# Kernel tuning notes

Hardware: AMD Instinct MI355X
Metric: run time of the kernel (lower is better)

The kernel has to match this reference:

```python
import jax, jax.numpy as jnp
import numpy as np

NEG_SLOPE = 0.2

def setup_inputs() -> dict:
    key = jax.random.key(0)
    k1, k2, k3, k4 = jax.random.split(key, 4)
    N, K, C_IN, C_OUT = 8192, 4, 512, 512
    inputs = jax.random.normal(k1, (N, C_IN), dtype=jnp.float32)
    adj_set = jax.random.uniform(k2, (K, N, N), dtype=jnp.float32)
    att = jax.random.uniform(k3, (K,), dtype=jnp.float32)
    # xavier_uniform for w
    limit = float(np.sqrt(6.0 / (C_IN + C_OUT)))
    w = jax.random.uniform(k4, (C_IN, C_OUT), minval=-limit, maxval=limit, dtype=jnp.float32)
    b = jnp.zeros((C_OUT,), dtype=jnp.float32)
    return {"inputs": inputs, "adj_set": adj_set, "att": att, "w": w, "b": b}

def reference(inputs, adj_set, att, w, b):
    # support: [N, C_out]
    support = inputs @ w + b
    # residual=True path: outputs = sum_i att[i] * (adj_i @ support)
    #                             = (sum_i att[i] * adj_i) @ support
    combined_adj = jnp.einsum('k,knm->nm', att, adj_set)  # [N, N]
    outputs = combined_adj @ support                       # [N, C_out]
    # LeakyReLU(negative_slope=0.2)
    return jnp.where(outputs >= 0, outputs, NEG_SLOPE * outputs)
```

## Files before the change

kernel.cpp:

```cpp
#include <hip/hip_runtime.h>

#define LP  40
#define LPB 40

typedef __attribute__((ext_vector_type(8))) short short8;
typedef __attribute__((ext_vector_type(4))) short short4t;
typedef __attribute__((ext_vector_type(4))) float f32x4;

__device__ __forceinline__ short f2bf(float f) {
  unsigned u = __builtin_bit_cast(unsigned, f);
  u += 0x7FFFu + ((u >> 16) & 1u);
  return (short)(u >> 16);
}

__device__ __forceinline__ float lrelu(float v) { return v >= 0.f ? v : 0.2f * v; }

__global__ __launch_bounds__(256) void k_wt(const float* __restrict__ w,
                                            short* __restrict__ wt) {
  __shared__ float t[64][65];
  int c0 = (blockIdx.x & 7) * 64;
  int n0 = (blockIdx.x >> 3) * 64;
  int r  = threadIdx.x >> 4;
  int q4 = (threadIdx.x & 15) * 4;
  for (int i = 0; i < 4; i++) {
    int c = r + i * 16;
    f32x4 v = *(const f32x4*)(w + (size_t)(c0 + c) * 512 + (n0 + q4));
    t[c][q4 + 0] = v[0]; t[c][q4 + 1] = v[1]; t[c][q4 + 2] = v[2]; t[c][q4 + 3] = v[3];
  }
  __syncthreads();
  for (int i = 0; i < 4; i++) {
    int n = r + i * 16;
    short4t o;
    for (int j = 0; j < 4; j++) o[j] = f2bf(t[q4 + j][n]);
    *(short4t*)(wt + (size_t)(n0 + n) * 512 + (c0 + q4)) = o;
  }
}

__global__ __launch_bounds__(512, 2) void k_support(const float* __restrict__ inp,
                                                    const short* __restrict__ wt,
                                                    const float* __restrict__ bias,
                                                    short* __restrict__ sup) {
  __shared__ __align__(16) short As[512 * LP];
  __shared__ __align__(16) short Bs[64 * LP];
  const int tid = threadIdx.x;
  const int m0 = blockIdx.x * 64;
  const int wave = tid >> 6, lane = tid & 63;
  const int wn = wave >> 1, wm = wave & 1;
  const int lr = lane & 15, lk = lane >> 4;
  const int bm = tid >> 3, bk = (tid & 7) * 4;
  f32x4 acc[8][2] = {};
  short8 ar[4]; f32x4 br;
  auto loadA = [&](int s) {
    const short* p = wt + (size_t)tid * 512 + s * 32;
    ar[0] = *(const short8*)(p);      ar[1] = *(const short8*)(p + 8);
    ar[2] = *(const short8*)(p + 16); ar[3] = *(const short8*)(p + 24);
  };
  auto loadB = [&](int s) {
    br = *(const f32x4*)(inp + (size_t)(m0 + bm) * 512 + s * 32 + bk);
  };
  loadA(0); loadB(0);
  for (int s = 0; s < 16; s++) {
    short* ad = As + tid * LP;
    *(short8*)(ad) = ar[0]; *(short8*)(ad + 8) = ar[1];
    *(short8*)(ad + 16) = ar[2]; *(short8*)(ad + 24) = ar[3];
    short4t bo;
    for (int j = 0; j < 4; j++) bo[j] = f2bf(br[j]);
    *(short4t*)(Bs + bm * LP + bk) = bo;
    __syncthreads();
    if (s + 1 < 16) { loadA(s + 1); loadB(s + 1); }
    short8 af[8], bfr[2];
    for (int nf = 0; nf < 8; nf++)
      af[nf] = *(const short8*)(As + (wn * 128 + nf * 16 + lr) * LP + lk * 8);
    for (int mf = 0; mf < 2; mf++)
      bfr[mf] = *(const short8*)(Bs + (wm * 32 + mf * 16 + lr) * LP + lk * 8);
    for (int nf = 0; nf < 8; nf++)
      for (int mf = 0; mf < 2; mf++)
        acc[nf][mf] = __builtin_amdgcn_mfma_f32_16x16x32_bf16(af[nf], bfr[mf], acc[nf][mf], 0, 0, 0);
    __syncthreads();
  }
  for (int nf = 0; nf < 8; nf++) {
    int nb = wn * 128 + nf * 16 + lk * 4;
    for (int mf = 0; mf < 2; mf++) {
      int m = m0 + wm * 32 + mf * 16 + lr;
      for (int j = 0; j < 4; j++) {
        int n = nb + j;
        sup[(size_t)n * 8192 + m] = f2bf(acc[nf][mf][j] + bias[n]);
      }
    }
  }
}

#define ISSUE(SL, S) {                                                          \
    const float* p_ = abase + (size_t)(S) * 32;                                 \
    R[SL][0] = __builtin_nontemporal_load((const f32x4*)(p_));                  \
    R[SL][1] = __builtin_nontemporal_load((const f32x4*)(p_ + (1ull << 26)));   \
    R[SL][2] = __builtin_nontemporal_load((const f32x4*)(p_ + (2ull << 26)));   \
    R[SL][3] = __builtin_nontemporal_load((const f32x4*)(p_ + (3ull << 26)));   \
  }

#define STEP(U) {                                                               \
    const int s_ = s0 + (U);                                                    \
    if (s_ + 3 < nsteps) ISSUE(((U) + 3) & 3, s_ + 3);                          \
    short8 af[4];                                                               \
    _Pragma("unroll") for (int nf = 0; nf < 4; nf++)                            \
      af[nf] = *(const short8*)(supp + (size_t)(nf * 16) * 8192 + (size_t)s_ * 32); \
    f32x4 c;                                                                    \
    _Pragma("unroll") for (int e = 0; e < 4; e++)                               \
      c[e] = t0 * R[(U)][0][e] + t1 * R[(U)][1][e]                              \
           + t2 * R[(U)][2][e] + t3 * R[(U)][3][e];                             \
    short4t o;                                                                  \
    _Pragma("unroll") for (int e = 0; e < 4; e++) o[e] = f2bf(c[e]);            \
    *(short4t*)(Bs[(U) & 1] + r * LPB + q * 4) = o;                             \
    __syncthreads();                                                            \
    short8 bfr[4];                                                              \
    _Pragma("unroll") for (int mf = 0; mf < 4; mf++)                            \
      bfr[mf] = *(const short8*)(Bs[(U) & 1] + (mf * 16 + lr) * LPB + lk * 8);  \
    _Pragma("unroll") for (int nf = 0; nf < 4; nf++)                            \
      _Pragma("unroll") for (int mf = 0; mf < 4; mf++)                          \
        acc[nf][mf] = __builtin_amdgcn_mfma_f32_16x16x32_bf16(af[nf], bfr[mf],  \
                                                              acc[nf][mf], 0, 0, 0); \
  }

__global__ __launch_bounds__(512, 2) void k_main(const float* __restrict__ adj,
                                                 const float* __restrict__ att,
                                                 const short* __restrict__ sup,
                                                 float* __restrict__ part,
                                                 float* __restrict__ outp,
                                                 int ksplit) {
  __shared__ __align__(16) short Bs[2][64 * LPB];
  const int tid = threadIdx.x;
  const int b = blockIdx.x;
  const int xpk = 8 / ksplit;
  const int xcd = b & 7;
  const int kc = xcd / xpk;
  const int m0 = ((b >> 3) * xpk + (xcd % xpk)) * 64;
  const int kchunk = 8192 / ksplit;
  const int nsteps = kchunk / 32;
  const int kbase = kc * kchunk;
  const float t0 = att[0], t1 = att[1], t2 = att[2], t3 = att[3];
  const int wave = tid >> 6, lane = tid & 63;
  const int lr = lane & 15, lk = lane >> 4;
  const int r = tid >> 3, q = tid & 7;
  f32x4 acc[4][4] = {};
  const float* abase = adj + (size_t)(m0 + r) * 8192 + kbase + q * 4;
  const short* supp = sup + (size_t)(wave * 64 + lr) * 8192 + kbase + lk * 8;
  f32x4 R[4][4];

  ISSUE(0, 0); ISSUE(1, 1); ISSUE(2, 2);
  for (int s0 = 0; s0 < nsteps; s0 += 4) {
    STEP(0) STEP(1) STEP(2) STEP(3)
  }

#pragma unroll
  for (int nf = 0; nf < 4; nf++) {
    int n = wave * 64 + nf * 16 + lk * 4;
#pragma unroll
    for (int mf = 0; mf < 4; mf++) {
      int m = m0 + mf * 16 + lr;
      f32x4 v = acc[nf][mf];
      if (ksplit == 1) {
        for (int j = 0; j < 4; j++) v[j] = lrelu(v[j]);
        __builtin_nontemporal_store(v, (f32x4*)(outp + (size_t)m * 512 + n));
      } else {
        __builtin_nontemporal_store(v, (f32x4*)(part + ((size_t)kc << 22) + (size_t)m * 512 + n));
      }
    }
  }
}

__global__ __launch_bounds__(256) void k_reduce(const float* __restrict__ part,
                                                float* __restrict__ outp, int ksplit) {
  const size_t total = (size_t)8192 * 512 / 4;
  for (size_t i = (size_t)blockIdx.x * 256 + threadIdx.x; i < total;
       i += (size_t)gridDim.x * 256) {
    f32x4 a = __builtin_nontemporal_load((const f32x4*)(part + i * 4));
    for (int k = 1; k < ksplit; k++) {
      f32x4 bv = __builtin_nontemporal_load((const f32x4*)(part + ((size_t)k << 22) + i * 4));
      for (int j = 0; j < 4; j++) a[j] += bv[j];
    }
    f32x4 v;
    for (int j = 0; j < 4; j++) v[j] = lrelu(a[j]);
    __builtin_nontemporal_store(v, (f32x4*)(outp + i * 4));
  }
}

extern "C" void kernel_launch(void* const* d_in, const int* in_sizes, int n_in,
                              void* d_out, int out_size, void* d_ws, size_t ws_size,
                              hipStream_t stream) {
  const float* inputs = (const float*)d_in[0];
  const float* adj    = (const float*)d_in[1];
  const float* att    = (const float*)d_in[2];
  const float* w      = (const float*)d_in[3];
  const float* bias   = (const float*)d_in[4];
  float* outp = (float*)d_out;

  char* ws = (char*)d_ws;
  short* sup  = (short*)(ws);
  short* wt   = (short*)(ws + (8u << 20));
  float* part = (float*)(ws + (9u << 20));

  const size_t base = (9ull << 20), psz = (1ull << 24);
  int ksplit = (ws_size >= base + 2 * psz) ? 2 : 1;

  k_wt<<<64, 256, 0, stream>>>(w, wt);
  k_support<<<128, 512, 0, stream>>>(inputs, wt, bias, sup);
  k_main<<<128 * ksplit, 512, 0, stream>>>(adj, att, sup, part, outp, ksplit);
  if (ksplit > 1) k_reduce<<<1024, 256, 0, stream>>>(part, outp, ksplit);
}
```

Measured before the change: 317.7 us.

## Prefetch support fragments and pin memory waits with explicit waitcnt scheduling

Loads of the bf16 support fragments move into a double-buffered register prefetch one step ahead. The adjacency prefetch distance drops from three steps to two, with wrap-around indexing in place of a guard branch. Manual s_waitcnt vmcnt/lgkmcnt, raw s_barrier and sched_barrier calls pin the ordering so MFMAs overlap outstanding global loads instead of stalling on compiler-inserted full waits. The hard-coded vmcnt values depend on the exact number of loads issued, and the wrapped prefetches fetch redundant data in the final steps.

```diff
diff --git a/kernel.cpp b/kernel.cpp
--- a/kernel.cpp
+++ b/kernel.cpp
@@ -98,27 +98,40 @@
     R[SL][3] = __builtin_nontemporal_load((const f32x4*)(p_ + (3ull << 26)));   \
   }
 
+#define ISSUEAF(SL, S) {                                                        \
+    const short* q_ = supp + (size_t)(S) * 32;                                  \
+    AF[SL][0] = *(const short8*)(q_);                                           \
+    AF[SL][1] = *(const short8*)(q_ + (size_t)16 * 8192);                       \
+    AF[SL][2] = *(const short8*)(q_ + (size_t)32 * 8192);                       \
+    AF[SL][3] = *(const short8*)(q_ + (size_t)48 * 8192);                       \
+  }
+
 #define STEP(U) {                                                               \
-    const int s_ = s0 + (U);                                                    \
-    if (s_ + 3 < nsteps) ISSUE(((U) + 3) & 3, s_ + 3);                          \
-    short8 af[4];                                                               \
-    _Pragma("unroll") for (int nf = 0; nf < 4; nf++)                            \
-      af[nf] = *(const short8*)(supp + (size_t)(nf * 16) * 8192 + (size_t)s_ * 32); \
-    f32x4 c;                                                                    \
+    ISSUE(((U) + 2) & 3, (s0 + (U) + 2) & (nsteps - 1))                         \
+    ISSUEAF(((U) + 1) & 1, (s0 + (U) + 1) & (nsteps - 1))                       \
+    __builtin_amdgcn_sched_barrier(0);                                          \
+    asm volatile("s_waitcnt vmcnt(20)" ::: "memory");                           \
+    __builtin_amdgcn_sched_barrier(0);                                          \
+    f32x4 c_;                                                                   \
     _Pragma("unroll") for (int e = 0; e < 4; e++)                               \
-      c[e] = t0 * R[(U)][0][e] + t1 * R[(U)][1][e]                              \
-           + t2 * R[(U)][2][e] + t3 * R[(U)][3][e];                             \
-    short4t o;                                                                  \
-    _Pragma("unroll") for (int e = 0; e < 4; e++) o[e] = f2bf(c[e]);            \
-    *(short4t*)(Bs[(U) & 1] + r * LPB + q * 4) = o;                             \
-    __syncthreads();                                                            \
+      c_[e] = t0 * R[(U) & 3][0][e] + t1 * R[(U) & 3][1][e]                     \
+            + t2 * R[(U) & 3][2][e] + t3 * R[(U) & 3][3][e];                    \
+    short4t o_;                                                                 \
+    _Pragma("unroll") for (int e = 0; e < 4; e++) o_[e] = f2bf(c_[e]);          \
+    *(short4t*)(Bs[(U) & 1] + r * LPB + q * 4) = o_;                            \
+    asm volatile("s_waitcnt lgkmcnt(0)" ::: "memory");                          \
+    __builtin_amdgcn_sched_barrier(0);                                          \
+    __builtin_amdgcn_s_barrier();                                               \
+    __builtin_amdgcn_sched_barrier(0);                                          \
     short8 bfr[4];                                                              \
     _Pragma("unroll") for (int mf = 0; mf < 4; mf++)                            \
       bfr[mf] = *(const short8*)(Bs[(U) & 1] + (mf * 16 + lr) * LPB + lk * 8);  \
+    asm volatile("s_waitcnt vmcnt(8)" ::: "memory");                            \
+    __builtin_amdgcn_sched_barrier(0);                                          \
     _Pragma("unroll") for (int nf = 0; nf < 4; nf++)                            \
       _Pragma("unroll") for (int mf = 0; mf < 4; mf++)                          \
-        acc[nf][mf] = __builtin_amdgcn_mfma_f32_16x16x32_bf16(af[nf], bfr[mf],  \
-                                                              acc[nf][mf], 0, 0, 0); \
+        acc[nf][mf] = __builtin_amdgcn_mfma_f32_16x16x32_bf16(AF[(U) & 1][nf],  \
+                          bfr[mf], acc[nf][mf], 0, 0, 0);                       \
   }
 
 __global__ __launch_bounds__(512, 2) void k_main(const float* __restrict__ adj,
@@ -145,8 +158,9 @@
   const float* abase = adj + (size_t)(m0 + r) * 8192 + kbase + q * 4;
   const short* supp = sup + (size_t)(wave * 64 + lr) * 8192 + kbase + lk * 8;
   f32x4 R[4][4];
-
-  ISSUE(0, 0); ISSUE(1, 1); ISSUE(2, 2);
+  short8 AF[2][4];
+
+  ISSUE(0, 0) ISSUEAF(0, 0) ISSUE(1, 1)
   for (int s0 = 0; s0 < nsteps; s0 += 4) {
     STEP(0) STEP(1) STEP(2) STEP(3)
   }
```

Result: faster. 308.1 us, median of 2 (-3.0%).
